# Kernel tuning notes

Measured on AMD Instinct MI355X. Metric: run time of the kernel, lower is better.

## Reference

```python
import jax, jax.numpy as jnp
import numpy as np

P = 20            # corr_patch_size: displacement offsets in [-10, 9]
B, C, H, W = 8, 64, 64, 192


def _leaky(x):
    return jax.nn.leaky_relu(x, 0.1)


def _conv3d(x, w, b, stride, pad, groups):
    y = jax.lax.conv_general_dilated(
        x, w, window_strides=(stride, stride, stride),
        padding=[(pad, pad)] * 3,
        dimension_numbers=('NCDHW', 'OIDHW', 'NCDHW'),
        feature_group_count=groups)
    return y + b[None, :, None, None, None]


def _block(x, dw_w, dw_b, pw_w, pw_b, stride):
    # depthwise 3x3x3 (strided) -> LeakyReLU -> pointwise 1x1x1 -> LeakyReLU
    x = _leaky(_conv3d(x, dw_w, dw_b, stride, 1, x.shape[1]))
    x = _leaky(_conv3d(x, pw_w, pw_b, 1, 0, 1))
    return x


def _correlation(rgb, depth):
    # SpatialCorrelationSampler(kernel_size=1, patch_size=P, stride=1):
    # corr[b, di, dj, y, x] = sum_c rgb[b,c,y,x] * depth[b,c, y+di-P//2, x+dj-P//2]
    pad_lo, pad_hi = P // 2, P - 1 - P // 2   # offsets -10 .. 9
    dp = jnp.pad(depth, ((0, 0), (0, 0), (pad_lo, pad_hi), (pad_lo, pad_hi)))
    rows = []
    for di in range(P):                       # structural loop over patch rows
        dh = dp[:, :, di:di + H, :]           # [B, C, H, W+P-1]
        # all P horizontal shifts at once: [B, P, C, H, W]
        win = jnp.stack([dh[:, :, :, dj:dj + W] for dj in range(P)], axis=1)
        rows.append(jnp.einsum('bchw,bpchw->bphw', rgb, win))
    return jnp.stack(rows, axis=1)            # [B, P, P, H, W]


def setup_inputs() -> dict:
    key = jax.random.key(0)
    ks = jax.random.split(key, 12)

    def rn(k, shape, scale=0.05):
        return jax.random.normal(k, shape, jnp.float32) * scale

    return {
        'rgb_branch': jax.random.normal(ks[0], (B, C, H, W), jnp.float32),
        'depth_branch': jax.random.normal(ks[1], (B, C, H, W), jnp.float32),
        'dw1_w': rn(ks[2], (20, 1, 3, 3, 3)), 'dw1_b': jnp.zeros((20,), jnp.float32),
        'pw1_w': rn(ks[3], (20, 20, 1, 1, 1)), 'pw1_b': jnp.zeros((20,), jnp.float32),
        'dw2_w': rn(ks[4], (20, 1, 3, 3, 3)), 'dw2_b': jnp.zeros((20,), jnp.float32),
        'pw2_w': rn(ks[5], (40, 20, 1, 1, 1)), 'pw2_b': jnp.zeros((40,), jnp.float32),
        'dw3_w': rn(ks[6], (40, 1, 3, 3, 3)), 'dw3_b': jnp.zeros((40,), jnp.float32),
        'pw3_w': rn(ks[7], (40, 40, 1, 1, 1)), 'pw3_b': jnp.zeros((40,), jnp.float32),
        'dw4_w': rn(ks[8], (40, 1, 3, 3, 3)), 'dw4_b': jnp.zeros((40,), jnp.float32),
        'pw4_w': rn(ks[9], (80, 40, 1, 1, 1)), 'pw4_b': jnp.zeros((80,), jnp.float32),
    }


def reference(rgb_branch, depth_branch,
              dw1_w, dw1_b, pw1_w, pw1_b,
              dw2_w, dw2_b, pw2_w, pw2_b,
              dw3_w, dw3_b, pw3_w, pw3_b,
              dw4_w, dw4_b, pw4_w, pw4_b):
    corr = _correlation(rgb_branch, depth_branch)          # [B,20,20,H,W]
    out = _block(corr, dw1_w, dw1_b, pw1_w, pw1_b, 1)      # [B,20,20,H,W]
    out = _block(out, dw2_w, dw2_b, pw2_w, pw2_b, 2)       # [B,40,10,H/2,W/2]
    out = _block(out, dw3_w, dw3_b, pw3_w, pw3_b, 1)
    out = _block(out, dw4_w, dw4_b, pw4_w, pw4_b, 2)       # [B,80,5,H/4,W/4]
    return out
```

## Files before the change

kernel.cpp:

```cpp
#include <hip/hip_runtime.h>
#include <cstdint>
#include <cstddef>


typedef unsigned short u16;
typedef _Float16 f16_t;
typedef __attribute__((ext_vector_type(2))) _Float16 half2_t;
typedef __attribute__((ext_vector_type(8))) _Float16 half8_t;
typedef __attribute__((ext_vector_type(4))) float f32x4;

static __device__ inline u16 f2h(float f) {
    union { f16_t h; u16 u; } v; v.h = (f16_t)f; return v.u;
}
static __device__ inline half2_t H2(uint32_t u) {
    union { uint32_t u; half2_t h; } v; v.u = u; return v.h;
}

#if __has_builtin(__builtin_amdgcn_fdot2)
static __device__ inline float FDOT2(half2_t a, half2_t b, float c) {
    return __builtin_amdgcn_fdot2(a, b, c, false);
}
#else
static __device__ inline float FDOT2(half2_t a, half2_t b, float c) {
    return fmaf((float)a.x, (float)b.x, fmaf((float)a.y, (float)b.y, c));
}
#endif

#if __has_builtin(__builtin_amdgcn_alignbit)
static __device__ inline uint32_t mkp(uint32_t lo, uint32_t hi) {
    return __builtin_amdgcn_alignbit(hi, lo, 16);
}
#else
static __device__ inline uint32_t mkp(uint32_t lo, uint32_t hi) {
    return (lo >> 16) | (hi << 16);
}
#endif

static __device__ inline uint32_t ldu(const u16* p) { return *(const uint32_t*)p; }

__global__ __launch_bounds__(256) void transpose_f16(
        const float* __restrict__ rgb, const float* __restrict__ dep,
        u16* __restrict__ rgbT, u16* __restrict__ depT) {
    const int bh = blockIdx.x;
    const float* src = blockIdx.y ? dep : rgb;
    u16* dst = blockIdx.y ? depT : rgbT;
    const int tid = threadIdx.x;
    const int b = bh >> 6, h = bh & 63;

    __shared__ u16 S[64 * 194];

    const float* srcb = src + (size_t)b * 786432 + (size_t)h * 192;
#pragma unroll
    for (int it = 0; it < 12; ++it) {
        const int idx = it * 256 + tid;
        const int c = idx / 48, w4 = idx - c * 48;
        const float4 v = *(const float4*)(srcb + (size_t)c * 12288 + 4 * w4);
        u16* sp = &S[c * 194 + 4 * w4];
        sp[0] = f2h(v.x); sp[1] = f2h(v.y); sp[2] = f2h(v.z); sp[3] = f2h(v.w);
    }
    __syncthreads();
    u16* dstb = dst + (size_t)bh * 192 * 64;
#pragma unroll
    for (int it = 0; it < 12; ++it) {
        const int idx = it * 256 + tid;
        const int w = idx >> 4, c4 = idx & 15;
        ushort4 o;
        o.x = S[(4 * c4 + 0) * 194 + w];
        o.y = S[(4 * c4 + 1) * 194 + w];
        o.z = S[(4 * c4 + 2) * 194 + w];
        o.w = S[(4 * c4 + 3) * 194 + w];
        *(ushort4*)(dstb + (size_t)w * 64 + 4 * c4) = o;
    }
}

__global__ __launch_bounds__(256) void corr_mfma(
        const u16* __restrict__ rgbT, const u16* __restrict__ depT,
        u16* __restrict__ out) {
    const int idx = blockIdx.x;
    const int band = idx & 7;
    const int j    = idx >> 3;
    const int dig  = j % 5;
    const int rest = j / 5;
    const int h    = band * 8 + (rest & 7);
    const int b    = rest >> 3;
    const int tid = threadIdx.x;
    const int lane = tid & 63, wave = tid >> 6;
    const int n = lane & 15, q = lane >> 4;
    const int w0base = wave * 48;

    __shared__ u16 D4[4][4080];

    const u16* Abase = rgbT + (size_t)(b * 64 + h) * 12288;
    half8_t a0[3], a1[3];
#pragma unroll
    for (int t = 0; t < 3; ++t) {
        const half8_t* Ap = (const half8_t*)(Abase + (size_t)(w0base + t * 16 + n) * 64 + q * 8);
        a0[t] = Ap[0];
        a1[t] = Ap[4];
    }

#pragma unroll
    for (int i = 0; i < 4; ++i) {
        const int di = dig * 4 + i;
        const int hd = h + di - 10;
        if (hd < 0 || hd >= 64) continue;

        const u16* Bbase = depT + (size_t)(b * 64 + hd) * 12288;
        half8_t B0[5], B1[5];
#pragma unroll
        for (int k = 0; k < 5; ++k) {
            const int u0 = w0base + (k - 1) * 16;
            if (u0 >= 0 && u0 <= 176) {
                const half8_t* Bp = (const half8_t*)(Bbase + (size_t)(u0 + n) * 64 + q * 8);
                B0[k] = Bp[0];
                B1[k] = Bp[4];
            } else {
                B0[k] = (half8_t)(f16_t)0.f;
                B1[k] = (half8_t)(f16_t)0.f;
            }
        }
#pragma unroll
        for (int t = 0; t < 3; ++t) {
            const int w0 = w0base + t * 16;
            f32x4 acc[3];
#pragma unroll
            for (int ut = 0; ut < 3; ++ut) {
                acc[ut].x = 0.f; acc[ut].y = 0.f; acc[ut].z = 0.f; acc[ut].w = 0.f;
            }
#pragma unroll
            for (int ut = 0; ut < 3; ++ut) {
                const int k = t + ut;
                acc[ut] = __builtin_amdgcn_mfma_f32_16x16x32_f16(a0[t], B0[k], acc[ut], 0, 0, 0);
                acc[ut] = __builtin_amdgcn_mfma_f32_16x16x32_f16(a1[t], B1[k], acc[ut], 0, 0, 0);
            }
#pragma unroll
            for (int ut = 0; ut < 3; ++ut) {
#pragma unroll
                for (int r = 0; r < 4; ++r) {
                    const int dj = 16 * ut + n - 4 * q - r - 6;
                    const int w = w0 + 4 * q + r;
                    if (dj >= 0 && dj < 20)
                        D4[i][w * 21 + (w >> 2) + dj] = f2h(acc[ut][r]);
                }
            }
        }
    }

#pragma unroll
    for (int i = 0; i < 4; ++i) {
        const int di = dig * 4 + i;
        const int hd = h + di - 10;
        const bool valid = (hd >= 0) && (hd < 64);
        u16* outb = out + ((size_t)((b * 20 + di) * 20) * 64 + h) * 192;
#pragma unroll
        for (int it = 0; it < 4; ++it) {
            const int item = it * 64 + lane;
            if (item < 240) {
                const int dj = item / 12;
                const int w4 = wave * 12 + (item - dj * 12);
                ushort4 o;
                if (valid) {
                    const int base = 85 * w4 + dj;
                    o.x = D4[i][base];
                    o.y = D4[i][base + 21];
                    o.z = D4[i][base + 42];
                    o.w = D4[i][base + 63];
                } else {
                    o = make_ushort4(0, 0, 0, 0);
                }
                *(ushort4*)(outb + (size_t)dj * 12288 + 4 * w4) = o;
            }
        }
    }
}

template<int CIN, int COUT, int S, int DT, int DIN, int HIN, int WIN,
         int DO, int HO, int WO, typename TOUT>
static __device__ __forceinline__ void fused_impl(
        const u16* __restrict__ x,
        const float* __restrict__ dw_w, const float* __restrict__ dw_b,
        const float* __restrict__ pw_w, const float* __restrict__ pw_b,
        TOUT* __restrict__ y) {
    static_assert(WO % 48 == 0 && HO % 4 == 0, "tile divisibility");
    constexpr int CINP = (CIN == 20) ? 22 : 42;
    constexpr int NTASK = CIN * 12;
    constexpr int WT = WO / 48;
    constexpr int NP = S * (DT - 1) + 3;
    constexpr int ROWS = 3 * S + 3;
    constexpr int NL = (S == 1) ? 4 : 5;
    constexpr int G  = (S == 1) ? 6 : 3;
    constexpr int NG = ROWS / G;

    const int wt = blockIdx.x % WT;
    const int ht = blockIdx.x / WT;
    const int d0 = blockIdx.y * DT;
    const int b  = blockIdx.z;
    const int tid = threadIdx.x;
    const int h0 = ht * 4;
    const int wbase = wt * 48;

    __shared__ float sDW[CIN * 27];
    __shared__ float sDB[CIN];
    __shared__ u16   sT[DT * 4 * 48 * CINP + 16];

    for (int i = tid; i < CIN * 27; i += 256) sDW[i] = dw_w[i];
    for (int i = tid; i < CIN; i += 256) sDB[i] = dw_b[i];
    __syncthreads();

    for (int idx = tid; idx < NTASK; idx += 256) {
        const int ci = idx / 12;
        const int wg = idx - ci * 12;
        const int w0g = wbase + wg * 4;
        const int offA = (w0g > 0) ? -2 : 0;

        half2_t KA[9], KB[9];
#pragma unroll
        for (int t = 0; t < 9; ++t) {
            const int kd = t / 3, kh = t - 3 * kd;
            const float k0 = sDW[ci * 27 + kd * 9 + kh * 3 + 0];
            const float k1 = sDW[ci * 27 + kd * 9 + kh * 3 + 1];
            const float k2 = sDW[ci * 27 + kd * 9 + kh * 3 + 2];
            half2_t a; a.x = (f16_t)k0; a.y = (f16_t)k1; KA[t] = a;
            half2_t bb;
            if constexpr (S == 1) { bb.x = (f16_t)k2; bb.y = (f16_t)0.f; }
            else                  { bb.x = (f16_t)0.f; bb.y = (f16_t)k2; }
            KB[t] = bb;
        }

        float acc[DT][4][4];
#pragma unroll
        for (int dl = 0; dl < DT; ++dl)
#pragma unroll
            for (int a = 0; a < 4; ++a)
#pragma unroll
                for (int c = 0; c < 4; ++c) acc[dl][a][c] = 0.f;

        const u16* plane0 = x + (size_t)(b * CIN + ci) * DIN * HIN * WIN;
#pragma unroll
        for (int p = 0; p < NP; ++p) {
            const int din = S * d0 - 1 + p;
            if (din < 0 || din >= DIN) continue;
            const u16* pl = plane0 + (size_t)din * HIN * WIN;
#pragma unroll
            for (int g = 0; g < NG; ++g) {
                uint32_t R[G][NL];
#pragma unroll
                for (int rr = 0; rr < G; ++rr) {
                    const int r = g * G + rr;
                    int hin = h0 * S - 1 + r;
                    int hc = hin < 0 ? 0 : (hin >= HIN ? HIN - 1 : hin);
                    const u16* rowp = pl + (size_t)hc * WIN + (size_t)w0g * S;
                    R[rr][0] = ldu(rowp + offA);
                    R[rr][1] = ldu(rowp);
                    R[rr][2] = ldu(rowp + 2);
                    R[rr][3] = ldu(rowp + 4);
                    if constexpr (S == 2) R[rr][4] = ldu(rowp + 6);
                }
#pragma unroll
                for (int rr = 0; rr < G; ++rr) {
                    const int r = g * G + rr;
                    const int hin = h0 * S - 1 + r;
                    uint32_t D0 = R[rr][0], D1 = R[rr][1];
                    uint32_t D2 = R[rr][2], D3 = R[rr][3];
                    uint32_t E4 = 0;
                    if constexpr (S == 2) E4 = R[rr][4];
                    D0 = (w0g > 0) ? D0 : 0u;
                    if constexpr (S == 1) D3 = (w0g + 4 < WIN) ? D3 : 0u;
                    if constexpr (S == 1) {
                        if (r == 0 || r == ROWS - 1) {
                            const bool rv = (hin >= 0) && (hin < HIN);
                            if (!rv) { D0 = 0; D1 = 0; D2 = 0; D3 = 0; }
                        }
                    } else {
                        if (r == 0) {
                            const bool rv = (hin >= 0);
                            if (!rv) { D0 = 0; D1 = 0; D2 = 0; D3 = 0; E4 = 0; }
                        }
                    }
                    uint32_t PA[4], PB[4];
                    if constexpr (S == 1) {
                        const uint32_t m01 = mkp(D0, D1);
                        const uint32_t m12 = mkp(D1, D2);
                        const uint32_t m23 = mkp(D2, D3);
                        PA[0] = m01; PA[1] = D1; PA[2] = m12; PA[3] = D2;
                        PB[0] = m12; PB[1] = D2; PB[2] = m23; PB[3] = D3;
                    } else {
                        PA[0] = mkp(D0, D1); PA[1] = mkp(D1, D2);
                        PA[2] = mkp(D2, D3); PA[3] = mkp(D3, E4);
                        PB[0] = D1; PB[1] = D2; PB[2] = D3; PB[3] = E4;
                    }
#pragma unroll
                    for (int dl = 0; dl < DT; ++dl) {
                        const int kd = p - S * dl;
                        if (kd < 0 || kd > 2) continue;
#pragma unroll
                        for (int hh = 0; hh < 4; ++hh) {
                            const int kh = r - S * hh;
                            if (kh < 0 || kh > 2) continue;
                            const int t = kd * 3 + kh;
#pragma unroll
                            for (int k = 0; k < 4; ++k)
                                acc[dl][hh][k] = FDOT2(H2(PB[k]), KB[t],
                                                 FDOT2(H2(PA[k]), KA[t],
                                                       acc[dl][hh][k]));
                        }
                    }
                }
            }
        }

        const float bia = sDB[ci];
#pragma unroll
        for (int dl = 0; dl < DT; ++dl) {
#pragma unroll
            for (int hh = 0; hh < 4; ++hh) {
#pragma unroll
                for (int k = 0; k < 4; ++k) {
                    const float t = acc[dl][hh][k] + bia;
                    sT[((dl * 4 + hh) * 48 + wg * 4 + k) * CINP + ci] =
                        f2h(fmaxf(t, 0.1f * t));
                }
            }
        }
    }
    __syncthreads();

    constexpr int NT = (COUT + 15) / 16;
    constexpr int KH = (CIN + 31) / 32;
    constexpr int MTW = DT * 3;
    const int lane = tid & 63, wave = tid >> 6;
    const int m15 = lane & 15, q = lane >> 4;

    half8_t bf[NT][KH];
    float   pb[NT];
#pragma unroll
    for (int nt = 0; nt < NT; ++nt) {
        const int co = nt * 16 + m15;
        pb[nt] = (co < COUT) ? pw_b[co] : 0.f;
#pragma unroll
        for (int kh = 0; kh < KH; ++kh) {
            union { half8_t v; f16_t e[8]; } u;
#pragma unroll
            for (int j = 0; j < 8; ++j) {
                const int ci = kh * 32 + q * 8 + j;
                u.e[j] = (co < COUT && ci < CIN)
                         ? (f16_t)pw_w[co * CIN + ci] : (f16_t)0.f;
            }
            bf[nt][kh] = u.v;
        }
    }

    const size_t planeSz = (size_t)DO * HO * WO;
    for (int mt = wave * MTW; mt < (wave + 1) * MTW; ++mt) {
        const int dl  = mt / 12;
        const int rem = mt - dl * 12;
        const int hh  = rem / 3;
        const int w0  = (rem - hh * 3) * 16;
        if (d0 + dl >= DO) continue;

        const int pos0 = (dl * 4 + hh) * 48 + w0 + m15;
        const u16* ap = &sT[(size_t)pos0 * CINP];
        union { uint32_t u[4]; half8_t v; } af[KH];
#pragma unroll
        for (int kh = 0; kh < KH; ++kh) {
            const int ci0 = kh * 32 + q * 8;
            af[kh].u[0] = (ci0     < CIN) ? ldu(ap + ci0)     : 0u;
            af[kh].u[1] = (ci0 + 2 < CIN) ? ldu(ap + ci0 + 2) : 0u;
            af[kh].u[2] = (ci0 + 4 < CIN) ? ldu(ap + ci0 + 4) : 0u;
            af[kh].u[3] = (ci0 + 6 < CIN) ? ldu(ap + ci0 + 6) : 0u;
        }
#pragma unroll
        for (int nt = 0; nt < NT; ++nt) {
            f32x4 acc;
            acc.x = 0.f; acc.y = 0.f; acc.z = 0.f; acc.w = 0.f;
#pragma unroll
            for (int kh = 0; kh < KH; ++kh)
                acc = __builtin_amdgcn_mfma_f32_16x16x32_f16(
                          af[kh].v, bf[nt][kh], acc, 0, 0, 0);
            const int co = nt * 16 + m15;
            if (co < COUT) {
                const float bias = pb[nt];
                TOUT* yp = y + (size_t)b * COUT * planeSz + (size_t)co * planeSz
                             + (size_t)(d0 + dl) * HO * WO
                             + (size_t)(h0 + hh) * WO + wbase + w0 + q * 4;
                float s0 = acc.x + bias, s1 = acc.y + bias;
                float s2 = acc.z + bias, s3 = acc.w + bias;
                s0 = fmaxf(s0, 0.1f * s0); s1 = fmaxf(s1, 0.1f * s1);
                s2 = fmaxf(s2, 0.1f * s2); s3 = fmaxf(s3, 0.1f * s3);
                if constexpr (sizeof(TOUT) == 4) {
                    float4 o; o.x = s0; o.y = s1; o.z = s2; o.w = s3;
                    *(float4*)yp = o;
                } else {
                    ushort4 o;
                    o.x = f2h(s0); o.y = f2h(s1); o.z = f2h(s2); o.w = f2h(s3);
                    *(ushort4*)yp = o;
                }
            }
        }
    }
}

__global__ __launch_bounds__(256) void fb1_dwpw(
        const u16* __restrict__ x, const float* __restrict__ dww,
        const float* __restrict__ dwb, const float* __restrict__ pww,
        const float* __restrict__ pwb, u16* __restrict__ y) {
    fused_impl<20, 20, 1, 4, 20, 64, 192, 20, 64, 192, u16>(x, dww, dwb, pww, pwb, y);
}
__global__ __launch_bounds__(256) void fb2_dwpw(
        const u16* __restrict__ x, const float* __restrict__ dww,
        const float* __restrict__ dwb, const float* __restrict__ pww,
        const float* __restrict__ pwb, u16* __restrict__ y) {
    fused_impl<20, 40, 2, 2, 20, 64, 192, 10, 32, 96, u16>(x, dww, dwb, pww, pwb, y);
}
__global__ __launch_bounds__(256) void fb3_dwpw(
        const u16* __restrict__ x, const float* __restrict__ dww,
        const float* __restrict__ dwb, const float* __restrict__ pww,
        const float* __restrict__ pwb, u16* __restrict__ y) {
    fused_impl<40, 40, 1, 2, 10, 32, 96, 10, 32, 96, u16>(x, dww, dwb, pww, pwb, y);
}
__global__ __launch_bounds__(256) void fb4_dwpw(
        const u16* __restrict__ x, const float* __restrict__ dww,
        const float* __restrict__ dwb, const float* __restrict__ pww,
        const float* __restrict__ pwb, float* __restrict__ y) {
    fused_impl<40, 80, 2, 1, 10, 32, 96, 5, 16, 48, float>(x, dww, dwb, pww, pwb, y);
}

extern "C" void kernel_launch(void* const* d_in, const int* in_sizes, int n_in,
                              void* d_out, int out_size, void* d_ws, size_t ws_size,
                              hipStream_t stream) {
    const float* rgb  = (const float*)d_in[0];
    const float* dep  = (const float*)d_in[1];
    const float* dw1w = (const float*)d_in[2];
    const float* dw1b = (const float*)d_in[3];
    const float* pw1w = (const float*)d_in[4];
    const float* pw1b = (const float*)d_in[5];
    const float* dw2w = (const float*)d_in[6];
    const float* dw2b = (const float*)d_in[7];
    const float* pw2w = (const float*)d_in[8];
    const float* pw2b = (const float*)d_in[9];
    const float* dw3w = (const float*)d_in[10];
    const float* dw3b = (const float*)d_in[11];
    const float* pw3w = (const float*)d_in[12];
    const float* pw3b = (const float*)d_in[13];
    const float* dw4w = (const float*)d_in[14];
    const float* dw4b = (const float*)d_in[15];
    const float* pw4w = (const float*)d_in[16];
    const float* pw4b = (const float*)d_in[17];

    const size_t HALF = 78643200;
    u16* corrO = (u16*)d_ws;
    u16* rgbT  = (u16*)((char*)d_ws + HALF);
    u16* depT  = (u16*)((char*)d_ws + HALF + 12582912);
    u16* b1o   = (u16*)((char*)d_ws + HALF);
    u16* b2o   = (u16*)d_ws;
    u16* b3o   = (u16*)((char*)d_ws + HALF);
    float* outp = (float*)d_out;

    transpose_f16<<<dim3(512, 2), 256, 0, stream>>>(rgb, dep, rgbT, depT);

    corr_mfma<<<dim3(2560), 256, 0, stream>>>(rgbT, depT, corrO);

    fb1_dwpw<<<dim3(64, 5, 8), 256, 0, stream>>>(corrO, dw1w, dw1b, pw1w, pw1b, b1o);
    fb2_dwpw<<<dim3(16, 5, 8), 256, 0, stream>>>(b1o, dw2w, dw2b, pw2w, pw2b, b2o);
    fb3_dwpw<<<dim3(16, 5, 8), 256, 0, stream>>>(b2o, dw3w, dw3b, pw3w, pw3b, b3o);
    fb4_dwpw<<<dim3(4, 5, 8), 256, 0, stream>>>(b3o, dw4w, dw4b, pw4w, pw4b, outp);
}
```

Baseline: 348.8 us.

## Prepack fp16 depthwise weights in LDS and raise occupancy for block 1

Depthwise weights are converted to packed half2 pairs once per block and stored in shared memory, so each task loads ready-made KA/KB values instead of converting floats itself. For the first fused block, the staging tile padding shrinks (CINP 20 instead of 22), the row group size drops from 6 to 3 to lower register pressure, and launch bounds request 5 blocks per SIMD-equivalent occupancy. Together these aim to raise occupancy and cut per-task setup work, at the risk of register spills or LDS bank conflicts from the unpadded stride.

```diff
diff --git a/kernel.cpp b/kernel.cpp
--- a/kernel.cpp
+++ b/kernel.cpp
@@ -182,13 +182,13 @@
         const float* __restrict__ pw_w, const float* __restrict__ pw_b,
         TOUT* __restrict__ y) {
     static_assert(WO % 48 == 0 && HO % 4 == 0, "tile divisibility");
-    constexpr int CINP = (CIN == 20) ? 22 : 42;
+    constexpr int CINP = (CIN == 20) ? ((S == 1 && DT == 4) ? 20 : 22) : 42;
     constexpr int NTASK = CIN * 12;
     constexpr int WT = WO / 48;
     constexpr int NP = S * (DT - 1) + 3;
     constexpr int ROWS = 3 * S + 3;
     constexpr int NL = (S == 1) ? 4 : 5;
-    constexpr int G  = (S == 1) ? 6 : 3;
+    constexpr int G  = 3;
     constexpr int NG = ROWS / G;
 
     const int wt = blockIdx.x % WT;
@@ -199,11 +199,23 @@
     const int h0 = ht * 4;
     const int wbase = wt * 48;
 
-    __shared__ float sDW[CIN * 27];
-    __shared__ float sDB[CIN];
-    __shared__ u16   sT[DT * 4 * 48 * CINP + 16];
-
-    for (int i = tid; i < CIN * 27; i += 256) sDW[i] = dw_w[i];
+    __shared__ uint32_t sKW[CIN * 18];
+    __shared__ float    sDB[CIN];
+    __shared__ u16      sT[DT * 4 * 48 * CINP + 16];
+
+    for (int i = tid; i < CIN * 9; i += 256) {
+        const int ci = i / 9, t = i - ci * 9;
+        const int kd = t / 3, kh = t - 3 * kd;
+        const float k0 = dw_w[ci * 27 + kd * 9 + kh * 3 + 0];
+        const float k1 = dw_w[ci * 27 + kd * 9 + kh * 3 + 1];
+        const float k2 = dw_w[ci * 27 + kd * 9 + kh * 3 + 2];
+        union { half2_t h; uint32_t u; } a, bb;
+        a.h.x = (f16_t)k0; a.h.y = (f16_t)k1;
+        if constexpr (S == 1) { bb.h.x = (f16_t)k2; bb.h.y = (f16_t)0.f; }
+        else                  { bb.h.x = (f16_t)0.f; bb.h.y = (f16_t)k2; }
+        sKW[ci * 18 + 2 * t]     = a.u;
+        sKW[ci * 18 + 2 * t + 1] = bb.u;
+    }
     for (int i = tid; i < CIN; i += 256) sDB[i] = dw_b[i];
     __syncthreads();
 
@@ -216,15 +228,8 @@
         half2_t KA[9], KB[9];
 #pragma unroll
         for (int t = 0; t < 9; ++t) {
-            const int kd = t / 3, kh = t - 3 * kd;
-            const float k0 = sDW[ci * 27 + kd * 9 + kh * 3 + 0];
-            const float k1 = sDW[ci * 27 + kd * 9 + kh * 3 + 1];
-            const float k2 = sDW[ci * 27 + kd * 9 + kh * 3 + 2];
-            half2_t a; a.x = (f16_t)k0; a.y = (f16_t)k1; KA[t] = a;
-            half2_t bb;
-            if constexpr (S == 1) { bb.x = (f16_t)k2; bb.y = (f16_t)0.f; }
-            else                  { bb.x = (f16_t)0.f; bb.y = (f16_t)k2; }
-            KB[t] = bb;
+            KA[t] = H2(sKW[ci * 18 + 2 * t]);
+            KB[t] = H2(sKW[ci * 18 + 2 * t + 1]);
         }
 
         float acc[DT][4][4];
@@ -400,7 +405,7 @@
     }
 }
 
-__global__ __launch_bounds__(256) void fb1_dwpw(
+__global__ __launch_bounds__(256, 5) void fb1_dwpw(
         const u16* __restrict__ x, const float* __restrict__ dww,
         const float* __restrict__ dwb, const float* __restrict__ pww,
         const float* __restrict__ pwb, u16* __restrict__ y) {
```

Result: slower. 364.5 us (+4.5%).
